# Kernel optimization log

Measured on AMD Instinct MI355X. Metric: run time of the kernel, lower is better.

Reference implementation:

```python
import jax, jax.numpy as jnp
from jax import lax
import numpy as np

DN = ('NCHW', 'OIHW', 'NCHW')

def conv2d_same(x, w, b):
    # 5x5, stride 1, pad 2 == SAME
    y = lax.conv_general_dilated(x, w, (1, 1), 'SAME', dimension_numbers=DN)
    return y + b[None, :, None, None]

def setup_inputs() -> dict:
    key = jax.random.key(0)
    ks = jax.random.split(key, 5)
    B, S, D = 8, 2048, 1024
    k55 = 0.2  # ~1/sqrt(25) init scale
    return {
        'x':  jax.random.normal(ks[0], (B, S, D), dtype=jnp.float32),
        'w1': jax.random.normal(ks[1], (1, 1, 5, 5), dtype=jnp.float32) * k55,
        'b1': jnp.zeros((1,), jnp.float32),
        'w2': jax.random.normal(ks[2], (1, 1, 5, 5), dtype=jnp.float32) * k55,
        'b2': jnp.zeros((1,), jnp.float32),
        'w3': jax.random.normal(ks[3], (1, 2, 5, 5), dtype=jnp.float32) * k55,
        'b3': jnp.zeros((1,), jnp.float32),
        'w4': jax.random.normal(ks[4], (1, 1, 5, 5), dtype=jnp.float32) * k55,
        'b4': jnp.zeros((1,), jnp.float32),
    }

def reference(x, w1, b1, w2, b2, w3, b3, w4, b4):
    # x: [b, s, d]
    xT = jnp.swapaxes(x, 1, 2)                              # [b, d, s]
    # self-similarity, softmax over BATCH dim (dim=0, as in original)
    NSSM = jax.nn.softmax(jnp.einsum('bsd,btd->bst', x, x), axis=0)   # [b, s, s]
    conv_x  = conv2d_same(x[:, None],  w1, b1)[:, 0]        # [b, s, d]
    conv_xT = conv2d_same(xT[:, None], w2, b2)[:, 0]        # [b, d, s]
    Attention_map = jax.nn.softmax(jnp.matmul(conv_x, conv_xT), axis=0)  # [b, s, s]
    Moca_map = conv2d_same(jnp.stack([NSSM, Attention_map], axis=1), w3, b3)[:, 0]  # [b, s, s]
    conv_g = conv2d_same(x[:, None], w4, b4)[:, 0]          # [b, s, d]
    Wz = jnp.matmul(Moca_map, conv_g)                       # [b, s, d]
    return Wz + x
```

## Files before the change

kernel.cpp:

```cpp
#include <hip/hip_runtime.h>

#define Bz 8
#define Sz 2048
#define Dz 1024

typedef __attribute__((ext_vector_type(8))) _Float16 f16x8;
typedef __attribute__((ext_vector_type(8))) short short8v;
typedef __attribute__((ext_vector_type(4))) short short4v;
typedef __attribute__((ext_vector_type(4))) float f32x4;

__device__ __forceinline__ short f2h(float f) {
    _Float16 h = (_Float16)f;
    return __builtin_bit_cast(short, h);
}
__device__ __forceinline__ float h2f(short s) {
    return (float)__builtin_bit_cast(_Float16, s);
}
__device__ __forceinline__ void gld16(const void* g, void* l) {
    __builtin_amdgcn_global_load_lds(
        (const __attribute__((address_space(1))) void*)g,
        (__attribute__((address_space(3))) void*)l, 16, 0, 0);
}

__global__ __launch_bounds__(256) void conv3_kernel(
    const float* __restrict__ x,
    const float* __restrict__ w1, const float* __restrict__ b1,
    const float* __restrict__ w2, const float* __restrict__ b2,
    short* __restrict__ x16, short* __restrict__ C1f, short* __restrict__ C2f)
{
    __shared__ float w[50];
    __shared__ float bias[2];
    const size_t SD = (size_t)Sz * Dz;
    int tid = threadIdx.x;
    if (tid < 25) w[tid] = w1[tid];
    else if (tid < 50) w[tid] = w2[tid - 25];
    if (tid == 50) { bias[0] = b1[0]; bias[1] = b2[0]; }
    __syncthreads();

    int d4 = tid * 4;
    int y = blockIdx.y;
    int s0 = (((y & 7) << 7) | (y >> 3)) * 2;
    int b = blockIdx.z;
    const float* xb = x + (size_t)b * SD + d4;

    float wv[6][12];
#pragma unroll
    for (int i = 0; i < 6; i++) {
        int ss = s0 + i - 2;
        int ssc = ss < 0 ? 0 : (ss >= Sz ? Sz - 1 : ss);
        const float* rp = xb + (size_t)ssc * Dz;
        if (d4 > 0) *(float4*)&wv[i][0] = *(const float4*)(rp - 4);
        else { wv[i][0] = wv[i][1] = wv[i][2] = wv[i][3] = 0.f; }
        *(float4*)&wv[i][4] = *(const float4*)rp;
        if (d4 < 1020) *(float4*)&wv[i][8] = *(const float4*)(rp + 4);
        else { wv[i][8] = wv[i][9] = wv[i][10] = wv[i][11] = 0.f; }
        if (ss != ssc) {
#pragma unroll
            for (int q = 0; q < 12; q++) wv[i][q] = 0.f;
        }
    }

#pragma unroll
    for (int r = 0; r < 2; r++) {
        float o1[4] = {}, o2[4] = {};
#pragma unroll
        for (int i = 0; i < 5; i++)
#pragma unroll
            for (int j = 0; j < 5; j++) {
                float c1w = w[i * 5 + j], c2w = w[25 + j * 5 + i];
#pragma unroll
                for (int q = 0; q < 4; q++) {
                    float v = wv[r + i][q + j + 2];
                    o1[q] = fmaf(c1w, v, o1[q]);
                    o2[q] = fmaf(c2w, v, o2[q]);
                }
            }
        size_t o = (size_t)b * SD + (size_t)(s0 + r) * Dz + d4;
        short4v hx, h1, h2;
#pragma unroll
        for (int q = 0; q < 4; q++) {
            hx[q] = f2h(wv[2 + r][q + 4]);
            h1[q] = f2h(o1[q] + bias[0]);
            h2[q] = f2h(o2[q] + bias[1]);
        }
        *(short4v*)(x16 + o) = hx;
        *(short4v*)(C1f + o) = h1;
        *(short4v*)(C2f + o) = h2;
    }
}

__global__ __launch_bounds__(256) void convT_kernel(
    const float* __restrict__ x, const float* __restrict__ w4,
    const float* __restrict__ b4, short* __restrict__ C4T)
{
    __shared__ float xs[68][73];
    __shared__ short ct[64][72];
    __shared__ float w[25];
    __shared__ float bb;
    const size_t SD = (size_t)Sz * Dz;
    int tid = threadIdx.x;
    if (tid < 25) w[tid] = w4[tid];
    if (tid == 25) bb = b4[0];

    int s0 = blockIdx.x * 64, d0 = blockIdx.y * 64, b = blockIdx.z;
    const float* xb = x + (size_t)b * SD;
    for (int k = tid; k < 68 * 68; k += 256) {
        int r = k / 68, c = k - r * 68;
        int gr = s0 - 2 + r, gc = d0 - 2 + c;
        float v = 0.f;
        if (gr >= 0 && gr < Sz && gc >= 0 && gc < Dz) v = xb[(size_t)gr * Dz + gc];
        xs[r][c] = v;
    }
    __syncthreads();

    int sl = tid & 63, dg = tid >> 6;
    float acc[16];
#pragma unroll
    for (int q = 0; q < 16; q++) acc[q] = bb;
#pragma unroll
    for (int i = 0; i < 5; i++) {
        float row[20];
#pragma unroll
        for (int m = 0; m < 20; m++) row[m] = xs[sl + i][dg * 16 + m];
#pragma unroll
        for (int j = 0; j < 5; j++) {
            float wv = w[i * 5 + j];
#pragma unroll
            for (int q = 0; q < 16; q++) acc[q] = fmaf(wv, row[q + j], acc[q]);
        }
    }
#pragma unroll
    for (int q = 0; q < 16; q++) ct[dg * 16 + q][sl] = f2h(acc[q]);
    __syncthreads();

    int dl = tid >> 2, sc = (tid & 3) * 16;
    f16x8 v0 = *(const f16x8*)&ct[dl][sc];
    f16x8 v1 = *(const f16x8*)&ct[dl][sc + 8];
    short* op = C4T + (size_t)b * SD + (size_t)(d0 + dl) * Sz + s0 + sc;
    *(f16x8*)op = v0;
    *(f16x8*)(op + 8) = v1;
}

__global__ __launch_bounds__(512, 2) void logit8_f16(
    const short* __restrict__ Ag, const short* __restrict__ Bg,
    const short* __restrict__ Aa, const short* __restrict__ Ba,
    short* __restrict__ Qg, short* __restrict__ Qa,
    int rlo, int sq256off, long PS)
{
    __shared__ char lds[131072];

    int flat = blockIdx.x + 8 * (blockIdx.y + 4 * blockIdx.z);
    int nid = (flat & 7) * 64 + (flat >> 3);
    int bx = nid & 7, by = (nid >> 3) & 3, bz = nid >> 5;
    const int map = bz >> 3, bzb = bz & 7;
    if (map == 0) {
        int ntl = bx - sq256off;
        if (ntl >= 0 && ntl < 4 && ntl < by) return;
    }

    const size_t SD = (size_t)Sz * Dz;
    const int K = Dz;
    const short* A = (map ? Aa : Ag) + (size_t)bzb * SD;
    const short* B = (map ? Ba : Bg) + (size_t)bzb * SD;
    short* Q = (map ? Qa : Qg) + (size_t)bzb * PS;

    const int m0 = by * 256, n0 = bx * 256;
    const int t = threadIdx.x;
    const int lane = t & 63;
    const int w = t >> 6;
    const int wm = w >> 2, wn = w & 3;
    const int fr = lane & 15;
    const int kb = lane >> 4;

    const int cc16 = ((t & 7) ^ ((t >> 3) & 7)) * 16;
    const int tr = t >> 3;
    const int bdst = (t >> 8) * 8192 + ((t >> 3) & 31) * 128 + (t & 7) * 16;

    auto STA = [&](int tile, int h) {
        char* base = lds + (tile & 1) * 65536;
#pragma unroll
        for (int j = 0; j < 2; j++) {
            int row = m0 + j * 128 + h * 64 + tr;
            gld16((const char*)A + ((size_t)row * K + tile * 64) * 2 + cc16,
                  base + j * 16384 + h * 8192 + t * 16);
        }
    };
    auto STB = [&](int tile, int h) {
        char* base = lds + (tile & 1) * 65536 + 32768;
#pragma unroll
        for (int j = 0; j < 2; j++) {
            int u = j * 64 + tr;
            int row = n0 + (u >> 5) * 64 + h * 32 + (u & 31);
            gld16((const char*)B + ((size_t)row * K + tile * 64) * 2 + cc16,
                  base + j * 16384 + h * 4096 + bdst);
        }
    };

    int aoff[2], boff[2];
#pragma unroll
    for (int ks = 0; ks < 2; ks++) {
        int slot = ((ks * 4 + kb) ^ (fr & 7)) * 16;
        aoff[ks] = (wm * 128 + fr) * 128 + slot;
        boff[ks] = (wn * 64 + fr) * 128 + slot;
    }

    f16x8 aR[8];
    f16x8 bR[2][4];
    f32x4 acc[8][4];
#pragma unroll
    for (int i = 0; i < 8; i++)
#pragma unroll
        for (int j = 0; j < 4; j++) acc[i][j] = (f32x4){0.f, 0.f, 0.f, 0.f};

    auto LDA = [&](int qa, int d) {
        const char* p = lds + d * 65536 + qa * 8192;
#pragma unroll
        for (int f = 0; f < 4; f++)
#pragma unroll
            for (int ks = 0; ks < 2; ks++)
                aR[f * 2 + ks] = *(const f16x8*)(p + aoff[ks] + f * 2048);
    };
    auto LDB = [&](int qb, int d, int which) {
        const char* p = lds + d * 65536 + 32768 + qb * 4096;
#pragma unroll
        for (int g = 0; g < 2; g++)
#pragma unroll
            for (int ks = 0; ks < 2; ks++)
                bR[which][g * 2 + ks] = *(const f16x8*)(p + boff[ks] + g * 2048);
    };
#define MMQ(qa, qb, which)                                                        \
    __builtin_amdgcn_s_setprio(1);                                                \
    _Pragma("unroll") for (int f = 0; f < 4; f++)                                 \
        _Pragma("unroll") for (int g = 0; g < 2; g++)                             \
            _Pragma("unroll") for (int ks = 0; ks < 2; ks++)                      \
                acc[(qa)*4 + f][(qb)*2 + g] = __builtin_amdgcn_mfma_f32_16x16x32_f16( \
                    aR[f * 2 + ks], bR[which][g * 2 + ks], acc[(qa)*4 + f][(qb)*2 + g], 0, 0, 0); \
    __builtin_amdgcn_s_setprio(0);

#define BAR()  __builtin_amdgcn_s_barrier(); __builtin_amdgcn_sched_barrier(0)
#define WAIT4() asm volatile("s_waitcnt vmcnt(4)" ::: "memory"); __builtin_amdgcn_sched_barrier(0)
#define WAIT0() asm volatile("s_waitcnt vmcnt(0)" ::: "memory"); __builtin_amdgcn_sched_barrier(0)

    STA(0, 0); STB(0, 0); STA(0, 1); STB(0, 1);
    STA(1, 0); STB(1, 0);

    const int NIT = K / 128;
    for (int it = 0; it < NIT - 1; ++it) {
        const int V = 2 * it + 1, W = 2 * it + 2, X = 2 * it + 3;
        WAIT4(); BAR();
        STA(V, 1); LDA(0, 0); LDB(0, 0, 0); MMQ(0, 0, 0);
        BAR();
        STB(V, 1); LDB(1, 0, 1); MMQ(0, 1, 1);
        BAR();
        STA(W, 0); LDA(1, 0); MMQ(1, 0, 0);
        BAR();
        STB(W, 0); MMQ(1, 1, 1);
        WAIT4(); BAR();
        STA(W, 1); LDA(0, 1); LDB(0, 1, 0); MMQ(0, 0, 0);
        BAR();
        STB(W, 1); LDB(1, 1, 1); MMQ(0, 1, 1);
        BAR();
        STA(X, 0); LDA(1, 1); MMQ(1, 0, 0);
        BAR();
        STB(X, 0); MMQ(1, 1, 1);
    }
    {
        const int V = 2 * NIT - 1;
        WAIT4(); BAR();
        STA(V, 1); LDA(0, 0); LDB(0, 0, 0); MMQ(0, 0, 0);
        BAR();
        STB(V, 1); LDB(1, 0, 1); MMQ(0, 1, 1);
        BAR();
        LDA(1, 0); MMQ(1, 0, 0);
        BAR();
        MMQ(1, 1, 1);
        WAIT0(); BAR();
        LDA(0, 1); LDB(0, 1, 0); MMQ(0, 0, 0);
        BAR();
        LDB(1, 1, 1); MMQ(0, 1, 1);
        BAR();
        LDA(1, 1); MMQ(1, 0, 0);
        BAR();
        MMQ(1, 1, 1);
    }
#undef MMQ
#undef BAR
#undef WAIT4
#undef WAIT0

#pragma unroll
    for (int mf = 0; mf < 8; mf++)
#pragma unroll
        for (int nf = 0; nf < 4; nf++) {
            int col = n0 + wn * 64 + nf * 16 + fr;
#pragma unroll
            for (int r = 0; r < 4; r++) {
                int rowg = m0 + wm * 128 + mf * 16 + kb * 4 + r;
                float o = acc[mf][nf][r];
                if (map == 0 && rlo + rowg == col) o -= 1024.f;
                Q[(size_t)rowg * Sz + col] = f2h(o);
            }
        }
}

__global__ __launch_bounds__(512, 2) void wz8_f16(
    const short* __restrict__ M0, const short* __restrict__ M1,
    const short* __restrict__ C4Tm,
    const float* __restrict__ X, float* __restrict__ Out,
    long psM0, long psM1)
{
    __shared__ char lds[131072];

    int flat = blockIdx.x + 4 * (blockIdx.y + 8 * blockIdx.z);
    int nid = (flat & 7) * 32 + (flat >> 3);
    int bx = nid & 3, by = (nid >> 2) & 7, bz = nid >> 5;

    const size_t SD = (size_t)Sz * Dz;
    const int K = Sz;
    const short* A0 = M0 + (size_t)bz * psM0;
    const short* A1 = M1 + (size_t)bz * psM1;
    const short* B = C4Tm + (size_t)bz * SD;
    const float* Src = X + (size_t)bz * SD;
    float* C = Out + (size_t)bz * SD;

    const int m0 = by * 256, n0 = bx * 256;
    const int t = threadIdx.x;
    const int lane = t & 63;
    const int w = t >> 6;
    const int wm = w >> 2, wn = w & 3;
    const int fr = lane & 15;
    const int kb = lane >> 4;

    const int cc16 = ((t & 7) ^ ((t >> 3) & 7)) * 16;
    const int tr = t >> 3;
    const int bdst = (t >> 8) * 8192 + ((t >> 3) & 31) * 128 + (t & 7) * 16;

    auto STA = [&](int tile, int h) {
        char* base = lds + (tile & 1) * 65536;
#pragma unroll
        for (int j = 0; j < 2; j++) {
            int row = m0 + j * 128 + h * 64 + tr;
            const short* src = (row < 1022) ? (A0 + (size_t)row * K)
                                            : (A1 + (size_t)(row - 1022) * K);
            gld16((const char*)src + (size_t)tile * 128 + cc16,
                  base + j * 16384 + h * 8192 + t * 16);
        }
    };
    auto STB = [&](int tile, int h) {
        char* base = lds + (tile & 1) * 65536 + 32768;
#pragma unroll
        for (int j = 0; j < 2; j++) {
            int u = j * 64 + tr;
            int row = n0 + (u >> 5) * 64 + h * 32 + (u & 31);
            gld16((const char*)B + ((size_t)row * K + tile * 64) * 2 + cc16,
                  base + j * 16384 + h * 4096 + bdst);
        }
    };

    int aoff[2], boff[2];
#pragma unroll
    for (int ks = 0; ks < 2; ks++) {
        int slot = ((ks * 4 + kb) ^ (fr & 7)) * 16;
        aoff[ks] = (wm * 128 + fr) * 128 + slot;
        boff[ks] = (wn * 64 + fr) * 128 + slot;
    }

    f16x8 aR[8];
    f16x8 bR[2][4];
    f32x4 acc[8][4];
#pragma unroll
    for (int i = 0; i < 8; i++)
#pragma unroll
        for (int j = 0; j < 4; j++) acc[i][j] = (f32x4){0.f, 0.f, 0.f, 0.f};

    auto LDA = [&](int qa, int d) {
        const char* p = lds + d * 65536 + qa * 8192;
#pragma unroll
        for (int f = 0; f < 4; f++)
#pragma unroll
            for (int ks = 0; ks < 2; ks++)
                aR[f * 2 + ks] = *(const f16x8*)(p + aoff[ks] + f * 2048);
    };
    auto LDB = [&](int qb, int d, int which) {
        const char* p = lds + d * 65536 + 32768 + qb * 4096;
#pragma unroll
        for (int g = 0; g < 2; g++)
#pragma unroll
            for (int ks = 0; ks < 2; ks++)
                bR[which][g * 2 + ks] = *(const f16x8*)(p + boff[ks] + g * 2048);
    };
#define MMQ(qa, qb, which)                                                        \
    __builtin_amdgcn_s_setprio(1);                                                \
    _Pragma("unroll") for (int f = 0; f < 4; f++)                                 \
        _Pragma("unroll") for (int g = 0; g < 2; g++)                             \
            _Pragma("unroll") for (int ks = 0; ks < 2; ks++)                      \
                acc[(qa)*4 + f][(qb)*2 + g] = __builtin_amdgcn_mfma_f32_16x16x32_f16( \
                    aR[f * 2 + ks], bR[which][g * 2 + ks], acc[(qa)*4 + f][(qb)*2 + g], 0, 0, 0); \
    __builtin_amdgcn_s_setprio(0);

#define BAR()  __builtin_amdgcn_s_barrier(); __builtin_amdgcn_sched_barrier(0)
#define WAIT4() asm volatile("s_waitcnt vmcnt(4)" ::: "memory"); __builtin_amdgcn_sched_barrier(0)
#define WAIT0() asm volatile("s_waitcnt vmcnt(0)" ::: "memory"); __builtin_amdgcn_sched_barrier(0)

    STA(0, 0); STB(0, 0); STA(0, 1); STB(0, 1);
    STA(1, 0); STB(1, 0);

    const int NIT = K / 128;
    for (int it = 0; it < NIT - 1; ++it) {
        const int V = 2 * it + 1, W = 2 * it + 2, X2 = 2 * it + 3;
        WAIT4(); BAR();
        STA(V, 1); LDA(0, 0); LDB(0, 0, 0); MMQ(0, 0, 0);
        BAR();
        STB(V, 1); LDB(1, 0, 1); MMQ(0, 1, 1);
        BAR();
        STA(W, 0); LDA(1, 0); MMQ(1, 0, 0);
        BAR();
        STB(W, 0); MMQ(1, 1, 1);
        WAIT4(); BAR();
        STA(W, 1); LDA(0, 1); LDB(0, 1, 0); MMQ(0, 0, 0);
        BAR();
        STB(W, 1); LDB(1, 1, 1); MMQ(0, 1, 1);
        BAR();
        STA(X2, 0); LDA(1, 1); MMQ(1, 0, 0);
        BAR();
        STB(X2, 0); MMQ(1, 1, 1);
    }
    {
        const int V = 2 * NIT - 1;
        WAIT4(); BAR();
        STA(V, 1); LDA(0, 0); LDB(0, 0, 0); MMQ(0, 0, 0);
        BAR();
        STB(V, 1); LDB(1, 0, 1); MMQ(0, 1, 1);
        BAR();
        LDA(1, 0); MMQ(1, 0, 0);
        BAR();
        MMQ(1, 1, 1);
        WAIT0(); BAR();
        LDA(0, 1); LDB(0, 1, 0); MMQ(0, 0, 0);
        BAR();
        LDB(1, 1, 1); MMQ(0, 1, 1);
        BAR();
        LDA(1, 1); MMQ(1, 0, 0);
        BAR();
        MMQ(1, 1, 1);
    }
#undef MMQ
#undef BAR
#undef WAIT4
#undef WAIT0

#pragma unroll
    for (int mf = 0; mf < 8; mf++)
#pragma unroll
        for (int nf = 0; nf < 4; nf++) {
            int col = n0 + wn * 64 + nf * 16 + fr;
#pragma unroll
            for (int r = 0; r < 4; r++) {
                int rowg = m0 + wm * 128 + mf * 16 + kb * 4 + r;
                C[(size_t)rowg * Dz + col] = acc[mf][nf][r] + Src[(size_t)rowg * Dz + col];
            }
        }
}

__global__ __launch_bounds__(256) void mirror_g(
    short* __restrict__ F, int o0, long PS)
{
    __shared__ short ts[128][136];
    int p = blockIdx.x, b = blockIdx.y;
    int mi = 1, base = 0;
    while (p >= base + mi) { base += mi; mi++; }
    int nt = p - base;
    short* Fb = F + (size_t)b * PS;
    int t = threadIdx.x;
    int rr = t >> 1, c0 = (t & 1) * 64;
    const short* src = Fb + (size_t)(nt * 128 + rr) * Sz + o0 + mi * 128 + c0;
#pragma unroll
    for (int j = 0; j < 8; j++)
        *(short8v*)&ts[rr][c0 + j * 8] = *(const short8v*)(src + j * 8);
    __syncthreads();
    short* dst = Fb + (size_t)(mi * 128 + rr) * Sz + o0 + nt * 128 + c0;
#pragma unroll
    for (int j = 0; j < 8; j++) {
        short8v v;
#pragma unroll
        for (int e = 0; e < 8; e++) v[e] = ts[c0 + j * 8 + e][rr];
        *(short8v*)(dst + j * 8) = v;
    }
}

__global__ __launch_bounds__(256) void softmax_ip(
    short* __restrict__ Qg, short* __restrict__ Qa, int nElem, long ps)
{
    int i8 = (blockIdx.x * 256 + threadIdx.x) * 8;
    if (i8 >= nElem) return;
    short* Q = blockIdx.z ? Qa : Qg;

    short8v v[Bz];
    float f[Bz][8];
#pragma unroll
    for (int b = 0; b < Bz; b++) {
        v[b] = *(const short8v*)(Q + i8 + (size_t)b * ps);
#pragma unroll
        for (int e = 0; e < 8; e++) f[b][e] = h2f(v[b][e]);
    }
#pragma unroll
    for (int e = 0; e < 8; e++) {
        float mx = f[0][e];
#pragma unroll
        for (int b = 1; b < Bz; b++) mx = fmaxf(mx, f[b][e]);
        float sum = 0.f;
#pragma unroll
        for (int b = 0; b < Bz; b++) { f[b][e] = __expf(f[b][e] - mx); sum += f[b][e]; }
        float inv = 1.f / sum;
#pragma unroll
        for (int b = 0; b < Bz; b++) v[b][e] = f2h(f[b][e] * inv);
    }
#pragma unroll
    for (int b = 0; b < Bz; b++)
        *(short8v*)(Q + i8 + (size_t)b * ps) = v[b];
}

__global__ __launch_bounds__(256) void slab_copy(
    const short* __restrict__ Fg, const short* __restrict__ Fa,
    short* __restrict__ slab, long PS)
{
    int idx = blockIdx.x * 256 + threadIdx.x;
    int e = idx * 8;
    int map = e >> 16;
    int rem = e & 65535;
    int b = rem >> 13;
    int rem2 = rem & 8191;
    int row = rem2 >> 11;
    int col = rem2 & 2047;
    const short* src = (map ? Fa : Fg) + (size_t)b * PS + (size_t)(1020 + row) * Sz + col;
    *(short8v*)(slab + e) = *(const short8v*)src;
}

__global__ __launch_bounds__(256) void moca_kernel(
    const short* __restrict__ Gs, const short* __restrict__ As,
    const short* __restrict__ slab,
    const float* __restrict__ w3, const float* __restrict__ b3,
    short* __restrict__ Mout,
    int o0, int rlo, int slabLo, long psIn, long psOut)
{
    __shared__ float w[50];
    __shared__ float bb;
    int tid = threadIdx.x;
    if (tid < 50) w[tid] = w3[tid];
    if (tid == 50) bb = b3[0];
    __syncthreads();

    int t8 = tid * 8;
    int so = blockIdx.y, b = blockIdx.z;
    int s = o0 + so;
    const short* Gp = Gs + (size_t)b * psIn;
    const short* Ap = As + (size_t)b * psIn;

    float acc[8];
#pragma unroll
    for (int q = 0; q < 8; q++) acc[q] = bb;

#pragma unroll
    for (int i = 0; i < 5; i++) {
        int sr = s + i - 2;
        if (sr < 0 || sr >= Sz) continue;
        const short *gp, *ap;
        size_t ro;
        if (sr >= rlo) { gp = Gp; ap = Ap; ro = (size_t)(sr - rlo) * Sz; }
        else {
            gp = slab + (size_t)b * 8192;
            ap = slab + 65536 + (size_t)b * 8192;
            ro = (size_t)(sr - slabLo) * Sz;
        }
        float gw[16], aw[16];
#pragma unroll
        for (int g = 0; g < 4; g++) {
            int c0 = t8 - 4 + g * 4;
            if (c0 >= 0 && c0 + 3 < Sz) {
                short4v gv = *(const short4v*)(gp + ro + c0);
                short4v av = *(const short4v*)(ap + ro + c0);
#pragma unroll
                for (int e = 0; e < 4; e++) { gw[g * 4 + e] = h2f(gv[e]); aw[g * 4 + e] = h2f(av[e]); }
            } else {
#pragma unroll
                for (int e = 0; e < 4; e++) { gw[g * 4 + e] = 0.f; aw[g * 4 + e] = 0.f; }
            }
        }
#pragma unroll
        for (int j = 0; j < 5; j++) {
            float wg = w[i * 5 + j], wa = w[25 + i * 5 + j];
#pragma unroll
            for (int q = 0; q < 8; q++)
                acc[q] = fmaf(wg, gw[q + j + 2], fmaf(wa, aw[q + j + 2], acc[q]));
        }
    }
    short4v r0, r1;
#pragma unroll
    for (int q = 0; q < 4; q++) { r0[q] = f2h(acc[q]); r1[q] = f2h(acc[q + 4]); }
    short* op = Mout + (size_t)b * psOut + (size_t)so * Sz + t8;
    *(short4v*)op = r0;
    *(short4v*)(op + 4) = r1;
}

extern "C" void kernel_launch(void* const* d_in, const int* in_sizes, int n_in,
                              void* d_out, int out_size, void* d_ws, size_t ws_size,
                              hipStream_t stream)
{
    const float* x  = (const float*)d_in[0];
    const float* w1 = (const float*)d_in[1];
    const float* b1 = (const float*)d_in[2];
    const float* w2 = (const float*)d_in[3];
    const float* b2 = (const float*)d_in[4];
    const float* w3 = (const float*)d_in[5];
    const float* b3 = (const float*)d_in[6];
    const float* w4 = (const float*)d_in[7];
    const float* b4 = (const float*)d_in[8];
    float* out = (float*)d_out;

    const size_t SD = (size_t)Sz * Dz;
    const size_t BSD2 = (size_t)Bz * SD * 2;

    char* ws = (char*)d_ws;
    short* x16 = (short*)(ws);
    short* C1f = (short*)(ws + 1 * BSD2);
    short* C2f = (short*)(ws + 2 * BSD2);
    short* C4T = (short*)(ws + 3 * BSD2);
    char* strip0 = ws + 4 * BSD2;

    const size_t PS   = (size_t)1024 * Sz;
    const size_t PSM0 = (size_t)1022 * Sz;
    const size_t PSM1 = (size_t)1026 * Sz;
    short* Fg   = (short*)strip0;
    short* Fa   = Fg + (size_t)Bz * PS;
    short* Mf0  = Fa + (size_t)Bz * PS;
    short* slab = Mf0 + (size_t)Bz * PSM0;
    short* Mf1  = x16;

    conv3_kernel<<<dim3(1, Sz / 2, Bz), 256, 0, stream>>>(
        x, w1, b1, w2, b2, x16, C1f, C2f);
    convT_kernel<<<dim3(Sz / 64, Dz / 64, Bz), 256, 0, stream>>>(x, w4, b4, C4T);

    const int ne = 1024 * Sz;

    logit8_f16<<<dim3(8, 4, 16), 512, 0, stream>>>(
        x16, x16, C1f, C2f, Fg, Fa, 0, 0, (long)PS);
    mirror_g<<<dim3(28, Bz), 256, 0, stream>>>(Fg, 0, (long)PS);
    softmax_ip<<<dim3((ne / 8 + 255) / 256, 1, 2), 256, 0, stream>>>(Fg, Fa, ne, (long)PS);
    slab_copy<<<dim3(64), 256, 0, stream>>>(Fg, Fa, slab, (long)PS);
    moca_kernel<<<dim3(1, 1022, Bz), 256, 0, stream>>>(
        Fg, Fa, slab, w3, b3, Mf0, 0, 0, 0, (long)PS, (long)PSM0);

    logit8_f16<<<dim3(8, 4, 16), 512, 0, stream>>>(
        x16 + (size_t)1024 * Dz, x16, C1f + (size_t)1024 * Dz, C2f,
        Fg, Fa, 1024, 4, (long)PS);
    mirror_g<<<dim3(28, Bz), 256, 0, stream>>>(Fg, 1024, (long)PS);
    softmax_ip<<<dim3((ne / 8 + 255) / 256, 1, 2), 256, 0, stream>>>(Fg, Fa, ne, (long)PS);
    moca_kernel<<<dim3(1, 1026, Bz), 256, 0, stream>>>(
        Fg, Fa, slab, w3, b3, Mf1, 1022, 1024, 1020, (long)PS, (long)PSM1);

    wz8_f16<<<dim3(4, 8, 8), 512, 0, stream>>>(
        Mf0, Mf1, C4T, x, out, (long)PSM0, (long)PSM1);
}
```

Measured before the change: 519.1 us.

## Fuse batch-dim softmax into Moca conv kernel, one output row per conv3 block

Removes the separate in-place softmax pass over both logit maps and instead computes the softmax over the batch dimension on the fly inside the Moca 5x5 conv. Each block now handles all 8 batches for a row, recomputing exp for the halo columns and the 5 neighbouring rows. This avoids a full read-modify-write of the two large fp16 maps, at the cost of redundant exp work and a large per-thread register footprint (8x8 accumulators plus 8x12 loaded values), which may lower occupancy. conv3_kernel also drops from two output rows per block to one, launching twice as many blocks.

```diff
diff --git a/kernel.cpp b/kernel.cpp
--- a/kernel.cpp
+++ b/kernel.cpp
@@ -39,14 +39,14 @@
 
     int d4 = tid * 4;
     int y = blockIdx.y;
-    int s0 = (((y & 7) << 7) | (y >> 3)) * 2;
+    int s = ((y & 7) << 8) | (y >> 3);
     int b = blockIdx.z;
     const float* xb = x + (size_t)b * SD + d4;
 
-    float wv[6][12];
-#pragma unroll
-    for (int i = 0; i < 6; i++) {
-        int ss = s0 + i - 2;
+    float wv[5][12];
+#pragma unroll
+    for (int i = 0; i < 5; i++) {
+        int ss = s + i - 2;
         int ssc = ss < 0 ? 0 : (ss >= Sz ? Sz - 1 : ss);
         const float* rp = xb + (size_t)ssc * Dz;
         if (d4 > 0) *(float4*)&wv[i][0] = *(const float4*)(rp - 4);
@@ -60,33 +60,30 @@
         }
     }
 
-#pragma unroll
-    for (int r = 0; r < 2; r++) {
-        float o1[4] = {}, o2[4] = {};
-#pragma unroll
-        for (int i = 0; i < 5; i++)
-#pragma unroll
-            for (int j = 0; j < 5; j++) {
-                float c1w = w[i * 5 + j], c2w = w[25 + j * 5 + i];
-#pragma unroll
-                for (int q = 0; q < 4; q++) {
-                    float v = wv[r + i][q + j + 2];
-                    o1[q] = fmaf(c1w, v, o1[q]);
-                    o2[q] = fmaf(c2w, v, o2[q]);
-                }
+    float o1[4] = {}, o2[4] = {};
+#pragma unroll
+    for (int i = 0; i < 5; i++)
+#pragma unroll
+        for (int j = 0; j < 5; j++) {
+            float c1w = w[i * 5 + j], c2w = w[25 + j * 5 + i];
+#pragma unroll
+            for (int q = 0; q < 4; q++) {
+                float v = wv[i][q + j + 2];
+                o1[q] = fmaf(c1w, v, o1[q]);
+                o2[q] = fmaf(c2w, v, o2[q]);
             }
-        size_t o = (size_t)b * SD + (size_t)(s0 + r) * Dz + d4;
-        short4v hx, h1, h2;
-#pragma unroll
-        for (int q = 0; q < 4; q++) {
-            hx[q] = f2h(wv[2 + r][q + 4]);
-            h1[q] = f2h(o1[q] + bias[0]);
-            h2[q] = f2h(o2[q] + bias[1]);
-        }
-        *(short4v*)(x16 + o) = hx;
-        *(short4v*)(C1f + o) = h1;
-        *(short4v*)(C2f + o) = h2;
-    }
+        }
+    size_t o = (size_t)b * SD + (size_t)s * Dz + d4;
+    short4v hx, h1, h2;
+#pragma unroll
+    for (int q = 0; q < 4; q++) {
+        hx[q] = f2h(wv[2][q + 4]);
+        h1[q] = f2h(o1[q] + bias[0]);
+        h2[q] = f2h(o2[q] + bias[1]);
+    }
+    *(short4v*)(x16 + o) = hx;
+    *(short4v*)(C1f + o) = h1;
+    *(short4v*)(C2f + o) = h2;
 }
 
 __global__ __launch_bounds__(256) void convT_kernel(
@@ -486,38 +483,6 @@
         for (int e = 0; e < 8; e++) v[e] = ts[c0 + j * 8 + e][rr];
         *(short8v*)(dst + j * 8) = v;
     }
-}
-
-__global__ __launch_bounds__(256) void softmax_ip(
-    short* __restrict__ Qg, short* __restrict__ Qa, int nElem, long ps)
-{
-    int i8 = (blockIdx.x * 256 + threadIdx.x) * 8;
-    if (i8 >= nElem) return;
-    short* Q = blockIdx.z ? Qa : Qg;
-
-    short8v v[Bz];
-    float f[Bz][8];
-#pragma unroll
-    for (int b = 0; b < Bz; b++) {
-        v[b] = *(const short8v*)(Q + i8 + (size_t)b * ps);
-#pragma unroll
-        for (int e = 0; e < 8; e++) f[b][e] = h2f(v[b][e]);
-    }
-#pragma unroll
-    for (int e = 0; e < 8; e++) {
-        float mx = f[0][e];
-#pragma unroll
-        for (int b = 1; b < Bz; b++) mx = fmaxf(mx, f[b][e]);
-        float sum = 0.f;
-#pragma unroll
-        for (int b = 0; b < Bz; b++) { f[b][e] = __expf(f[b][e] - mx); sum += f[b][e]; }
-        float inv = 1.f / sum;
-#pragma unroll
-        for (int b = 0; b < Bz; b++) v[b][e] = f2h(f[b][e] * inv);
-    }
-#pragma unroll
-    for (int b = 0; b < Bz; b++)
-        *(short8v*)(Q + i8 + (size_t)b * ps) = v[b];
 }
 
 __global__ __launch_bounds__(256) void slab_copy(
@@ -536,8 +501,8 @@
     *(short8v*)(slab + e) = *(const short8v*)src;
 }
 
-__global__ __launch_bounds__(256) void moca_kernel(
-    const short* __restrict__ Gs, const short* __restrict__ As,
+__global__ __launch_bounds__(256) void moca_sm(
+    const short* __restrict__ Fg, const short* __restrict__ Fa,
     const short* __restrict__ slab,
     const float* __restrict__ w3, const float* __restrict__ b3,
     short* __restrict__ Mout,
@@ -551,55 +516,79 @@
     __syncthreads();
 
     int t8 = tid * 8;
-    int so = blockIdx.y, b = blockIdx.z;
+    int so = blockIdx.y;
     int s = o0 + so;
-    const short* Gp = Gs + (size_t)b * psIn;
-    const short* Ap = As + (size_t)b * psIn;
-
-    float acc[8];
-#pragma unroll
-    for (int q = 0; q < 8; q++) acc[q] = bb;
-
-#pragma unroll
+
+    float acc[8][8];
+#pragma unroll
+    for (int b = 0; b < 8; b++)
+#pragma unroll
+        for (int q = 0; q < 8; q++) acc[b][q] = bb;
+
     for (int i = 0; i < 5; i++) {
         int sr = s + i - 2;
         if (sr < 0 || sr >= Sz) continue;
-        const short *gp, *ap;
-        size_t ro;
-        if (sr >= rlo) { gp = Gp; ap = Ap; ro = (size_t)(sr - rlo) * Sz; }
-        else {
-            gp = slab + (size_t)b * 8192;
-            ap = slab + 65536 + (size_t)b * 8192;
-            ro = (size_t)(sr - slabLo) * Sz;
-        }
-        float gw[16], aw[16];
-#pragma unroll
-        for (int g = 0; g < 4; g++) {
-            int c0 = t8 - 4 + g * 4;
-            if (c0 >= 0 && c0 + 3 < Sz) {
-                short4v gv = *(const short4v*)(gp + ro + c0);
-                short4v av = *(const short4v*)(ap + ro + c0);
-#pragma unroll
-                for (int e = 0; e < 4; e++) { gw[g * 4 + e] = h2f(gv[e]); aw[g * 4 + e] = h2f(av[e]); }
-            } else {
-#pragma unroll
-                for (int e = 0; e < 4; e++) { gw[g * 4 + e] = 0.f; aw[g * 4 + e] = 0.f; }
+        bool inP = (sr >= rlo);
+#pragma unroll
+        for (int m = 0; m < 2; m++) {
+            const short* base;
+            long bstr;
+            if (inP) { base = (m ? Fa : Fg) + (size_t)(sr - rlo) * Sz; bstr = psIn; }
+            else     { base = slab + m * 65536 + (size_t)(sr - slabLo) * 2048; bstr = 8192; }
+
+            float lg[8][12];
+#pragma unroll
+            for (int b = 0; b < 8; b++) {
+                const short* p = base + (size_t)b * bstr;
+                short4v v1_ = (short4v){0, 0, 0, 0}, v4_ = (short4v){0, 0, 0, 0};
+                if (t8 >= 4) v1_ = *(const short4v*)(p + t8 - 4);
+                short4v v2_ = *(const short4v*)(p + t8);
+                short4v v3_ = *(const short4v*)(p + t8 + 4);
+                if (t8 + 8 < Sz) v4_ = *(const short4v*)(p + t8 + 8);
+                lg[b][0] = h2f(v1_[2]); lg[b][1] = h2f(v1_[3]);
+#pragma unroll
+                for (int e = 0; e < 4; e++) {
+                    lg[b][2 + e] = h2f(v2_[e]);
+                    lg[b][6 + e] = h2f(v3_[e]);
+                }
+                lg[b][10] = h2f(v4_[0]); lg[b][11] = h2f(v4_[1]);
             }
-        }
-#pragma unroll
-        for (int j = 0; j < 5; j++) {
-            float wg = w[i * 5 + j], wa = w[25 + i * 5 + j];
-#pragma unroll
-            for (int q = 0; q < 8; q++)
-                acc[q] = fmaf(wg, gw[q + j + 2], fmaf(wa, aw[q + j + 2], acc[q]));
-        }
-    }
-    short4v r0, r1;
-#pragma unroll
-    for (int q = 0; q < 4; q++) { r0[q] = f2h(acc[q]); r1[q] = f2h(acc[q + 4]); }
-    short* op = Mout + (size_t)b * psOut + (size_t)so * Sz + t8;
-    *(short4v*)op = r0;
-    *(short4v*)(op + 4) = r1;
+#pragma unroll
+            for (int k = 0; k < 12; k++) {
+                int c = t8 - 2 + k;
+                float mx = lg[0][k];
+#pragma unroll
+                for (int b = 1; b < 8; b++) mx = fmaxf(mx, lg[b][k]);
+                float sum = 0.f;
+#pragma unroll
+                for (int b = 0; b < 8; b++) {
+                    float e_ = __expf(lg[b][k] - mx);
+                    lg[b][k] = e_;
+                    sum += e_;
+                }
+                float inv = (c >= 0 && c < Sz) ? 1.f / sum : 0.f;
+#pragma unroll
+                for (int b = 0; b < 8; b++) lg[b][k] *= inv;
+            }
+#pragma unroll
+            for (int j = 0; j < 5; j++) {
+                float wgt = w[m * 25 + i * 5 + j];
+#pragma unroll
+                for (int b = 0; b < 8; b++)
+#pragma unroll
+                    for (int q = 0; q < 8; q++)
+                        acc[b][q] = fmaf(wgt, lg[b][q + j], acc[b][q]);
+            }
+        }
+    }
+
+#pragma unroll
+    for (int b = 0; b < 8; b++) {
+        short8v r;
+#pragma unroll
+        for (int q = 0; q < 8; q++) r[q] = f2h(acc[b][q]);
+        *(short8v*)(Mout + (size_t)b * psOut + (size_t)so * Sz + t8) = r;
+    }
 }
 
 extern "C" void kernel_launch(void* const* d_in, const int* in_sizes, int n_in,
@@ -636,26 +625,22 @@
     short* slab = Mf0 + (size_t)Bz * PSM0;
     short* Mf1  = x16;
 
-    conv3_kernel<<<dim3(1, Sz / 2, Bz), 256, 0, stream>>>(
+    conv3_kernel<<<dim3(1, Sz, Bz), 256, 0, stream>>>(
         x, w1, b1, w2, b2, x16, C1f, C2f);
     convT_kernel<<<dim3(Sz / 64, Dz / 64, Bz), 256, 0, stream>>>(x, w4, b4, C4T);
-
-    const int ne = 1024 * Sz;
 
     logit8_f16<<<dim3(8, 4, 16), 512, 0, stream>>>(
         x16, x16, C1f, C2f, Fg, Fa, 0, 0, (long)PS);
     mirror_g<<<dim3(28, Bz), 256, 0, stream>>>(Fg, 0, (long)PS);
-    softmax_ip<<<dim3((ne / 8 + 255) / 256, 1, 2), 256, 0, stream>>>(Fg, Fa, ne, (long)PS);
     slab_copy<<<dim3(64), 256, 0, stream>>>(Fg, Fa, slab, (long)PS);
-    moca_kernel<<<dim3(1, 1022, Bz), 256, 0, stream>>>(
+    moca_sm<<<dim3(1, 1022, 1), 256, 0, stream>>>(
         Fg, Fa, slab, w3, b3, Mf0, 0, 0, 0, (long)PS, (long)PSM0);
 
     logit8_f16<<<dim3(8, 4, 16), 512, 0, stream>>>(
         x16 + (size_t)1024 * Dz, x16, C1f + (size_t)1024 * Dz, C2f,
         Fg, Fa, 1024, 4, (long)PS);
     mirror_g<<<dim3(28, Bz), 256, 0, stream>>>(Fg, 1024, (long)PS);
-    softmax_ip<<<dim3((ne / 8 + 255) / 256, 1, 2), 256, 0, stream>>>(Fg, Fa, ne, (long)PS);
-    moca_kernel<<<dim3(1, 1026, Bz), 256, 0, stream>>>(
+    moca_sm<<<dim3(1, 1026, 1), 256, 0, stream>>>(
         Fg, Fa, slab, w3, b3, Mf1, 1022, 1024, 1020, (long)PS, (long)PSM1);
 
     wz8_f16<<<dim3(4, 8, 8), 512, 0, stream>>>(
```

Result: slower. 588.4 us (+13.4%).
